# Performance work log

Hardware: AMD Instinct MI355X
Metric: run time of the kernel (lower is better)

## Reference

```python
import jax, jax.numpy as jnp
import numpy as np

H = 2048          # hidden_size
I_MOE = 1408      # moe_intermediate_size (per expert)
I_SH = 5632       # shared_expert_intermediate_size
E = 8             # num_experts
TOP_K = 2         # num_experts_per_tok
B, S = 1, 2048


def setup_inputs() -> dict:
    key = jax.random.key(0)
    ks = jax.random.split(key, 7)
    sc = 0.02
    return {
        "hidden_states": jax.random.normal(ks[0], (B, S, H), jnp.float32),
        "W_router": jax.random.normal(ks[1], (E, H), jnp.float32) * sc,      # gate.weight
        "W_sgate": jax.random.normal(ks[2], (1, H), jnp.float32) * sc,       # shared_expert_gate.weight
        "Ws_gate_up": jax.random.normal(ks[3], (H, 2 * I_SH), jnp.float32) * sc,  # shared expert merged gate/up
        "Ws_down": jax.random.normal(ks[4], (I_SH, H), jnp.float32) * sc,
        "We_gate_up": jax.random.normal(ks[5], (E, H, 2 * I_MOE), jnp.float32) * sc,  # stacked expert gate/up
        "We_down": jax.random.normal(ks[6], (E, I_MOE, H), jnp.float32) * sc,
    }


def _silu_and_mul(gu, inter):
    # gate_up layout: [..., 2*inter] -> silu(gate) * up, matching SiluAndMul
    return jax.nn.silu(gu[..., :inter]) * gu[..., inter:]


def reference(hidden_states, W_router, W_sgate, Ws_gate_up, Ws_down, We_gate_up, We_down):
    orig_shape = hidden_states.shape
    x = hidden_states.reshape(-1, H)                     # [T, H]
    T = x.shape[0]

    # --- router: softmax in fp32 then top-k (NOT renormalized, as in source) ---
    logits = x @ W_router.T                              # [T, E]
    probs = jax.nn.softmax(logits.astype(jnp.float32), axis=-1)
    rw, sel = jax.lax.top_k(probs, TOP_K)                # [T, K]
    rw = rw.astype(x.dtype)

    # sparse combine matrix [T, E]: routing weight where selected, else 0
    combine = jnp.zeros((T, E), x.dtype).at[jnp.arange(T)[:, None], sel].add(rw)

    # --- shared expert ---
    sh = _silu_and_mul(x @ Ws_gate_up, I_SH) @ Ws_down    # [T, H]
    shared_out = sh * jax.nn.sigmoid(x @ W_sgate.T)       # [T, H]

    # --- experts: dense dispatch (math-identical to gather/MLP/index_add loop) ---
    gu = jnp.einsum('th,ehi->eti', x, We_gate_up)         # [E, T, 2*I_MOE]
    h = _silu_and_mul(gu, I_MOE)                          # [E, T, I_MOE]
    eo = jnp.einsum('eti,eih->eth', h, We_down)           # [E, T, H]
    sparse_out = jnp.einsum('eth,te->th', eo, combine)    # [T, H]

    return (shared_out + sparse_out).reshape(orig_shape)
```

## Files before the change

### kernel.cpp

```cpp
#include <hip/hip_runtime.h>
#include <cstdio>


#define H_DIM 2048
#define IMOE  1408
#define ISH   5632
#define NEXP  8
#define T_TOK 2048
#define TK_TOT (T_TOK * 2)

typedef __attribute__((ext_vector_type(8))) short short8;
typedef __attribute__((ext_vector_type(8))) __bf16 bf16x8;
typedef __attribute__((ext_vector_type(4))) float f32x4;

__device__ __forceinline__ float bf2f(unsigned short u) {
  union { unsigned int i; float f; } v; v.i = ((unsigned int)u) << 16; return v.f;
}
__device__ __forceinline__ unsigned short f2bf(float f) {
  union { float f; unsigned int i; } v; v.f = f;
  unsigned int x = v.i;
  return (unsigned short)((x + 0x7fffu + ((x >> 16) & 1u)) >> 16);
}

__device__ __forceinline__ f32x4 MFMA16(short8 a, short8 b, f32x4 c) {
  return __builtin_amdgcn_mfma_f32_16x16x32_bf16(
      __builtin_bit_cast(bf16x8, a), __builtin_bit_cast(bf16x8, b), c, 0, 0, 0);
}

__device__ __forceinline__ void gload_lds16(const unsigned short* g, unsigned short* l) {
  __builtin_amdgcn_global_load_lds(
      (const __attribute__((address_space(1))) unsigned int*)g,
      (__attribute__((address_space(3))) unsigned int*)l, 16, 0, 0);
}

__device__ __forceinline__ float silu_f(float x) { return x / (1.0f + __expf(-x)); }

#define SBAR()   asm volatile("s_barrier" ::: "memory")
#define VMCNT(n) asm volatile("s_waitcnt vmcnt(" #n ")" ::: "memory")


template <bool ILV>
__global__ __launch_bounds__(256)
void transpose_cvt_kernel(const float* __restrict__ src, unsigned short* __restrict__ dst,
                          int R, int C, int I, long sStride, long dStride) {
  src += (long)blockIdx.z * sStride;
  dst += (long)blockIdx.z * dStride;
  __shared__ float tile[32][33];
  int tx = threadIdx.x, ty = threadIdx.y;
  int x = blockIdx.x * 32 + tx;
  int yb = blockIdx.y * 32;
#pragma unroll
  for (int j = 0; j < 4; j++) {
    int y = yb + ty + j * 8;
    tile[ty + j * 8][tx] = src[(long)y * C + x];
  }
  __syncthreads();
  int r = yb + tx;
#pragma unroll
  for (int j = 0; j < 4; j++) {
    int c = blockIdx.x * 32 + ty + j * 8;
    int cd = ILV ? (c < I ? 2 * c : 2 * (c - I) + 1) : c;
    dst[(long)cd * R + r] = f2bf(tile[tx][ty + j * 8]);
  }
}

__global__ __launch_bounds__(256)
void cvt_x_kernel(const float* __restrict__ x, unsigned short* __restrict__ xb, int total4) {
  int i = blockIdx.x * 256 + threadIdx.x;
  if (i >= total4) return;
  float4 v = ((const float4*)x)[i];
  ushort4 o;
  o.x = f2bf(v.x); o.y = f2bf(v.y); o.z = f2bf(v.z); o.w = f2bf(v.w);
  ((ushort4*)xb)[i] = o;
}


__global__ __launch_bounds__(256)
void router_kernel(const float* __restrict__ x, const float* __restrict__ Wr,
                   const float* __restrict__ Wsg, float* __restrict__ rw,
                   int* __restrict__ sel, float* __restrict__ sgate_sig,
                   int* __restrict__ counts) {
  int t = blockIdx.x;
  const float* xr = x + (long)t * H_DIM;
  float p[9];
#pragma unroll
  for (int e = 0; e < 9; e++) p[e] = 0.0f;
  for (int h = threadIdx.x; h < H_DIM; h += 256) {
    float xv = xr[h];
#pragma unroll
    for (int e = 0; e < 8; e++) p[e] += xv * Wr[e * H_DIM + h];
    p[8] += xv * Wsg[h];
  }
#pragma unroll
  for (int e = 0; e < 9; e++)
    for (int off = 32; off > 0; off >>= 1)
      p[e] += __shfl_down(p[e], off, 64);
  __shared__ float red[4][9];
  int wave = threadIdx.x >> 6, lane = threadIdx.x & 63;
  if (lane == 0) {
#pragma unroll
    for (int e = 0; e < 9; e++) red[wave][e] = p[e];
  }
  __syncthreads();
  if (threadIdx.x == 0) {
    float lg[9];
#pragma unroll
    for (int e = 0; e < 9; e++) lg[e] = red[0][e] + red[1][e] + red[2][e] + red[3][e];
    float m = lg[0];
#pragma unroll
    for (int e = 1; e < 8; e++) m = fmaxf(m, lg[e]);
    float pr[8], s = 0.0f;
#pragma unroll
    for (int e = 0; e < 8; e++) { pr[e] = expf(lg[e] - m); s += pr[e]; }
    float inv = 1.0f / s;
#pragma unroll
    for (int e = 0; e < 8; e++) pr[e] *= inv;
    int i0 = 0;
#pragma unroll
    for (int e = 1; e < 8; e++) if (pr[e] > pr[i0]) i0 = e;
    int i1 = (i0 == 0) ? 1 : 0;
#pragma unroll
    for (int e = 0; e < 8; e++) if (e != i0 && pr[e] > pr[i1]) i1 = e;
    rw[t * 2] = pr[i0]; rw[t * 2 + 1] = pr[i1];
    sel[t * 2] = i0;    sel[t * 2 + 1] = i1;
    sgate_sig[t] = 1.0f / (1.0f + expf(-lg[8]));
    atomicAdd(&counts[i0], 1);
    atomicAdd(&counts[i1], 1);
  }
}

__global__ void scan_kernel(const int* __restrict__ counts, int* __restrict__ offsets) {
  if (threadIdx.x == 0 && blockIdx.x == 0) {
    int s = 0;
    for (int e = 0; e < NEXP; e++) { offsets[e] = s; s += counts[e]; }
    offsets[NEXP] = s;
  }
}

__global__ __launch_bounds__(256)
void scatter_kernel(const int* __restrict__ sel, const int* __restrict__ offsets,
                    int* __restrict__ cursor, int* __restrict__ tok_of_slot,
                    int* __restrict__ slot_of_tok) {
  int t = blockIdx.x * 256 + threadIdx.x;
  if (t >= T_TOK) return;
#pragma unroll
  for (int k = 0; k < 2; k++) {
    int e = sel[t * 2 + k];
    int pos = atomicAdd(&cursor[e], 1);
    int slot = offsets[e] + pos;
    tok_of_slot[slot] = t;
    slot_of_tok[t * 2 + k] = slot;
  }
}

__global__ __launch_bounds__(256)
void gather_kernel(const unsigned short* __restrict__ xbf, const int* __restrict__ tok,
                   unsigned short* __restrict__ xg) {
  int i = blockIdx.x * 256 + threadIdx.x;
  int slot = i >> 8, c8 = i & 255;
  long src = (long)tok[slot] * H_DIM + c8 * 8;
  ulonglong2 v = *(const ulonglong2*)(xbf + src);
  ((ulonglong2*)xg)[i] = v;
}

template <int EPI, bool EXPERT, bool GATHER>
__global__ __launch_bounds__(512, 2)
void gemm8_kernel(const unsigned short* __restrict__ A,
                  const unsigned short* __restrict__ BT,
                  void* __restrict__ Cv,
                  int N, int Kld, int KLEN, int M,
                  const int* __restrict__ counts, const int* __restrict__ offsets,
                  const int* __restrict__ tok_of_slot,
                  const float* __restrict__ rowscale, long bt_estride) {
  __shared__ unsigned short lds8[65536];

  int cnt = M, rowbase = 0, k0 = 0;
  const unsigned short* bt = BT;
  if constexpr (EXPERT) {
    int e = blockIdx.z;
    cnt = counts[e];
    rowbase = offsets[e];
    bt += (long)e * bt_estride;
  } else {
    k0 = blockIdx.z * KLEN;
  }
  int row0 = blockIdx.x * 256;
  if (row0 >= cnt) return;
  int col0 = blockIdx.y * 256;

  int tid = threadIdx.x, wave = tid >> 6, lane = tid & 63;
  int NT = KLEN / 32;

  const unsigned short* aSrc[2];
  const unsigned short* bSrc[2];
#pragma unroll
  for (int i = 0; i < 2; i++) {
    int r = i * 128 + (tid >> 2);
    int sw = (((tid & 3) ^ ((r >> 1) & 3)) * 8);
    long arow;
    if constexpr (EXPERT) {
      int s = rowbase + min(row0 + r, cnt - 1);
      arow = GATHER ? tok_of_slot[s] : s;
    } else {
      arow = row0 + r;
    }
    aSrc[i] = A + arow * (long)Kld + k0 + sw;
    bSrc[i] = bt + (long)(col0 + r) * Kld + k0 + sw;
  }
  int dA0 = wave * 512, dA1 = 4096 + wave * 512;
  int dB0 = 8192 + wave * 512, dB1 = 12288 + wave * 512;

  auto STAGE_A = [&](int u) {
    int b2 = (u & 3) * 16384;
    long kk = (long)min(u, NT - 1) * 32;
    gload_lds16(aSrc[0] + kk, &lds8[b2 + dA0]);
    gload_lds16(aSrc[1] + kk, &lds8[b2 + dA1]);
  };
  auto STAGE_B = [&](int u) {
    int b2 = (u & 3) * 16384;
    long kk = (long)min(u, NT - 1) * 32;
    gload_lds16(bSrc[0] + kk, &lds8[b2 + dB0]);
    gload_lds16(bSrc[1] + kk, &lds8[b2 + dB1]);
  };

  int wr = wave >> 2, wc = wave & 3;
  int fr = lane & 15, fg = lane >> 4;
  int addrA0[4], addrA1[4], addrB[4];
#pragma unroll
  for (int m = 0; m < 4; m++) {
    int rl0 = wr * 128 + m * 16 + fr;
    int rl1 = rl0 + 64;
    int cl  = wc * 64 + m * 16 + fr;
    addrA0[m] = rl0 * 32 + ((fg ^ ((rl0 >> 1) & 3)) * 8);
    addrA1[m] = rl1 * 32 + ((fg ^ ((rl1 >> 1) & 3)) * 8);
    addrB[m]  = 8192 + cl * 32 + ((fg ^ ((cl >> 1) & 3)) * 8);
  }

  STAGE_A(0); STAGE_B(0);
  STAGE_A(1); STAGE_B(1);
  STAGE_A(2); STAGE_B(2);
  VMCNT(8);
  SBAR();

  f32x4 acc[8][4] = {};

  for (int t = 0; t < NT; t++) {
    int b = (t & 3) * 16384;
    int u = t + 3;
    short8 Bf[4], Af[4];
#pragma unroll
    for (int n = 0; n < 4; n++) Bf[n] = *(const short8*)&lds8[b + addrB[n]];
#pragma unroll
    for (int m = 0; m < 4; m++) Af[m] = *(const short8*)&lds8[b + addrA0[m]];
    STAGE_A(u);
    SBAR();
    __builtin_amdgcn_s_setprio(1);
#pragma unroll
    for (int m = 0; m < 4; m++)
#pragma unroll
      for (int n = 0; n < 4; n++)
        acc[m][n] = MFMA16(Af[m], Bf[n], acc[m][n]);
    __builtin_amdgcn_s_setprio(0);
    SBAR();
#pragma unroll
    for (int m = 0; m < 4; m++) Af[m] = *(const short8*)&lds8[b + addrA1[m]];
    STAGE_B(u);
    SBAR();
    __builtin_amdgcn_s_setprio(1);
#pragma unroll
    for (int m = 0; m < 4; m++)
#pragma unroll
      for (int n = 0; n < 4; n++)
        acc[4 + m][n] = MFMA16(Af[m], Bf[n], acc[4 + m][n]);
    __builtin_amdgcn_s_setprio(0);
    VMCNT(8);
    SBAR();
  }
  VMCNT(0);

  int rowguard = cnt - row0;
#pragma unroll
  for (int mq = 0; mq < 8; mq++) {
    int rl = wr * 128 + (mq >> 2) * 64 + (mq & 3) * 16 + fg * 4;
#pragma unroll
    for (int n = 0; n < 4; n++) {
      int cg = col0 + wc * 64 + n * 16 + fr;
      f32x4 v = acc[mq][n];
#pragma unroll
      for (int j = 0; j < 4; j++) {
        int r = rl + j;
        float pv = __shfl_xor(v[j], 1);
        if (r < rowguard) {
          long orow = (long)rowbase + row0 + r;
          if constexpr (EPI == 1) {
            unsafeAtomicAdd(&((float*)Cv)[orow * (long)N + cg], v[j] * rowscale[orow]);
          } else if constexpr (EPI == 2) {
            ((float*)Cv)[orow * (long)N + cg] = v[j];
          } else {
            if (!(fr & 1)) {
              float hval = silu_f(v[j]) * pv;
              ((unsigned short*)Cv)[orow * (long)(N >> 1) + (cg >> 1)] = f2bf(hval);
            }
          }
        }
      }
    }
  }
}


__global__ __launch_bounds__(256)
void combine_kernel(float* __restrict__ out, const float* __restrict__ eo,
                    const int* __restrict__ slot_of_tok, const float* __restrict__ rw) {
  int i = blockIdx.x * 256 + threadIdx.x;
  const int h4n = H_DIM / 4;
  if (i >= T_TOK * h4n) return;
  int t = i / h4n;
  int h4 = i - t * h4n;
  int s0 = slot_of_tok[t * 2], s1 = slot_of_tok[t * 2 + 1];
  float w0 = rw[t * 2], w1 = rw[t * 2 + 1];
  float4 o = ((float4*)out)[i];
  float4 a = ((const float4*)eo)[(long)s0 * h4n + h4];
  float4 b = ((const float4*)eo)[(long)s1 * h4n + h4];
  o.x += w0 * a.x + w1 * b.x;
  o.y += w0 * a.y + w1 * b.y;
  o.z += w0 * a.z + w1 * b.z;
  o.w += w0 * a.w + w1 * b.w;
  ((float4*)out)[i] = o;
}


extern "C" void kernel_launch(void* const* d_in, const int* in_sizes, int n_in,
                              void* d_out, int out_size, void* d_ws, size_t ws_size,
                              hipStream_t stream) {
  (void)in_sizes; (void)n_in; (void)out_size;
  const float* x    = (const float*)d_in[0];
  const float* Wr   = (const float*)d_in[1];
  const float* Wsg  = (const float*)d_in[2];
  const float* Wsgu = (const float*)d_in[3];
  const float* Wsd  = (const float*)d_in[4];
  const float* Wegu = (const float*)d_in[5];
  const float* Wed  = (const float*)d_in[6];
  float* out = (float*)d_out;

  char* ws = (char*)d_ws;
  size_t off = 0;
  auto alloc = [&](size_t b) { size_t o = off; off += (b + 255) & ~(size_t)255; return o; };

  size_t o_xbf   = alloc((size_t)T_TOK * H_DIM * 2);
  size_t o_WsguT = alloc((size_t)2 * ISH * H_DIM * 2);
  size_t o_WsdT  = alloc((size_t)H_DIM * ISH * 2);
  size_t o_WeguT = alloc((size_t)NEXP * 2 * IMOE * H_DIM * 2);
  size_t o_WedT  = alloc((size_t)NEXP * H_DIM * IMOE * 2);
  size_t o_hsh   = alloc((size_t)T_TOK * ISH * 2);
  size_t o_he    = alloc((size_t)TK_TOT * IMOE * 2);
  size_t o_xg    = alloc((size_t)TK_TOT * H_DIM * 2);
  size_t o_ints  = alloc(256);
  size_t o_rw    = alloc((size_t)TK_TOT * 4);
  size_t o_sel   = alloc((size_t)TK_TOT * 4);
  size_t o_sg    = alloc((size_t)T_TOK * 4);
  size_t o_tok   = alloc((size_t)TK_TOT * 4);
  size_t o_s2t   = alloc((size_t)TK_TOT * 4);

  if (off > ws_size) {
    fprintf(stderr, "[moe kernel] workspace too small: need %zu have %zu\n", off, ws_size);
    return;
  }

  unsigned short* xbf   = (unsigned short*)(ws + o_xbf);
  unsigned short* WsguT = (unsigned short*)(ws + o_WsguT);
  unsigned short* WsdT  = (unsigned short*)(ws + o_WsdT);
  unsigned short* WeguT = (unsigned short*)(ws + o_WeguT);
  unsigned short* WedT  = (unsigned short*)(ws + o_WedT);
  unsigned short* h_sh  = (unsigned short*)(ws + o_hsh);
  unsigned short* h_e   = (unsigned short*)(ws + o_he);
  unsigned short* xg    = (unsigned short*)(ws + o_xg);
  float* eo             = (float*)(ws + o_WsguT);

  int* ints    = (int*)(ws + o_ints);
  int* counts  = ints;
  int* cursor  = ints + 8;
  int* offsets = ints + 16;
  float* rw    = (float*)(ws + o_rw);
  int* sel     = (int*)(ws + o_sel);
  float* sgate = (float*)(ws + o_sg);
  int* tok     = (int*)(ws + o_tok);
  int* s2t     = (int*)(ws + o_s2t);

  dim3 tb(32, 8, 1);

  hipMemsetAsync(ints, 0, 64, stream);
  hipMemsetAsync(out, 0, (size_t)T_TOK * H_DIM * 4, stream);

  transpose_cvt_kernel<true><<<dim3(2 * ISH / 32, H_DIM / 32, 1), tb, 0, stream>>>(
      Wsgu, WsguT, H_DIM, 2 * ISH, ISH, 0, 0);
  transpose_cvt_kernel<false><<<dim3(H_DIM / 32, ISH / 32, 1), tb, 0, stream>>>(
      Wsd, WsdT, ISH, H_DIM, 0, 0, 0);
  transpose_cvt_kernel<true><<<dim3(2 * IMOE / 32, H_DIM / 32, NEXP), tb, 0, stream>>>(
      Wegu, WeguT, H_DIM, 2 * IMOE, IMOE, (long)H_DIM * 2 * IMOE, (long)2 * IMOE * H_DIM);
  transpose_cvt_kernel<false><<<dim3(H_DIM / 32, IMOE / 32, NEXP), tb, 0, stream>>>(
      Wed, WedT, IMOE, H_DIM, 0, (long)IMOE * H_DIM, (long)H_DIM * IMOE);

  cvt_x_kernel<<<(T_TOK * H_DIM / 4) / 256, 256, 0, stream>>>(x, xbf, T_TOK * H_DIM / 4);

  router_kernel<<<T_TOK, 256, 0, stream>>>(x, Wr, Wsg, rw, sel, sgate, counts);
  scan_kernel<<<1, 64, 0, stream>>>(counts, offsets);
  scatter_kernel<<<(T_TOK + 255) / 256, 256, 0, stream>>>(sel, offsets, cursor, tok, s2t);
  gather_kernel<<<TK_TOT, 256, 0, stream>>>(xbf, tok, xg);

  gemm8_kernel<3, false, false><<<dim3(T_TOK / 256, 2 * ISH / 256, 1), 512, 0, stream>>>(
      xbf, WsguT, h_sh, 2 * ISH, H_DIM, H_DIM, T_TOK,
      nullptr, nullptr, nullptr, nullptr, 0);

  gemm8_kernel<3, true, false><<<dim3(T_TOK / 256, 2 * IMOE / 256, NEXP), 512, 0, stream>>>(
      xg, WeguT, h_e, 2 * IMOE, H_DIM, H_DIM, 0,
      counts, offsets, nullptr, nullptr, (long)2 * IMOE * H_DIM);

  gemm8_kernel<1, false, false><<<dim3(T_TOK / 256, H_DIM / 256, 4), 512, 0, stream>>>(
      h_sh, WsdT, out, H_DIM, ISH, ISH / 4, T_TOK,
      nullptr, nullptr, nullptr, sgate, 0);

  gemm8_kernel<2, true, false><<<dim3(T_TOK / 256, H_DIM / 256, NEXP), 512, 0, stream>>>(
      h_e, WedT, eo, H_DIM, IMOE, IMOE, 0,
      counts, offsets, nullptr, nullptr, (long)H_DIM * IMOE);

  combine_kernel<<<(T_TOK * H_DIM / 4) / 256, 256, 0, stream>>>(out, eo, s2t, rw);
}
```

Measured before the change: 797.5 us.

## Rewrite GEMM main loop as double-buffered BK=64 pipeline and interleave weight transposes

```diff
diff --git a/kernel.cpp b/kernel.cpp
--- a/kernel.cpp
+++ b/kernel.cpp
@@ -163,15 +163,14 @@
   ((ulonglong2*)xg)[i] = v;
 }
 
-template <int EPI, bool EXPERT, bool GATHER>
+template <int EPI, bool EXPERT>
 __global__ __launch_bounds__(512, 2)
-void gemm8_kernel(const unsigned short* __restrict__ A,
-                  const unsigned short* __restrict__ BT,
-                  void* __restrict__ Cv,
-                  int N, int Kld, int KLEN, int M,
-                  const int* __restrict__ counts, const int* __restrict__ offsets,
-                  const int* __restrict__ tok_of_slot,
-                  const float* __restrict__ rowscale, long bt_estride) {
+void gemm2p_kernel(const unsigned short* __restrict__ A,
+                   const unsigned short* __restrict__ BT,
+                   void* __restrict__ Cv,
+                   int N, int Kld, int KLEN, int M,
+                   const int* __restrict__ counts, const int* __restrict__ offsets,
+                   const float* __restrict__ rowscale, long bt_estride) {
   __shared__ unsigned short lds8[65536];
 
   int cnt = M, rowbase = 0, k0 = 0;
@@ -189,103 +188,75 @@
   int col0 = blockIdx.y * 256;
 
   int tid = threadIdx.x, wave = tid >> 6, lane = tid & 63;
-  int NT = KLEN / 32;
-
-  const unsigned short* aSrc[2];
-  const unsigned short* bSrc[2];
-#pragma unroll
-  for (int i = 0; i < 2; i++) {
-    int r = i * 128 + (tid >> 2);
-    int sw = (((tid & 3) ^ ((r >> 1) & 3)) * 8);
-    long arow;
-    if constexpr (EXPERT) {
-      int s = rowbase + min(row0 + r, cnt - 1);
-      arow = GATHER ? tok_of_slot[s] : s;
-    } else {
-      arow = row0 + r;
-    }
-    aSrc[i] = A + arow * (long)Kld + k0 + sw;
-    bSrc[i] = bt + (long)(col0 + r) * Kld + k0 + sw;
-  }
-  int dA0 = wave * 512, dA1 = 4096 + wave * 512;
-  int dB0 = 8192 + wave * 512, dB1 = 12288 + wave * 512;
-
-  auto STAGE_A = [&](int u) {
-    int b2 = (u & 3) * 16384;
-    long kk = (long)min(u, NT - 1) * 32;
-    gload_lds16(aSrc[0] + kk, &lds8[b2 + dA0]);
-    gload_lds16(aSrc[1] + kk, &lds8[b2 + dA1]);
-  };
-  auto STAGE_B = [&](int u) {
-    int b2 = (u & 3) * 16384;
-    long kk = (long)min(u, NT - 1) * 32;
-    gload_lds16(bSrc[0] + kk, &lds8[b2 + dB0]);
-    gload_lds16(bSrc[1] + kk, &lds8[b2 + dB1]);
-  };
+  int NT = KLEN / 64;
+
+  const unsigned short* aSrc[4];
+  const unsigned short* bSrc[4];
+#pragma unroll
+  for (int s = 0; s < 4; s++) {
+    int r = s * 64 + (tid >> 3);
+    int g = (tid & 7) ^ (r & 7);
+    long ar = row0 + r;
+    if (ar > cnt - 1) ar = cnt - 1;
+    ar += rowbase;
+    aSrc[s] = A + ar * (long)Kld + k0 + g * 8;
+    bSrc[s] = bt + (long)(col0 + r) * Kld + k0 + g * 8;
+  }
 
   int wr = wave >> 2, wc = wave & 3;
   int fr = lane & 15, fg = lane >> 4;
-  int addrA0[4], addrA1[4], addrB[4];
-#pragma unroll
-  for (int m = 0; m < 4; m++) {
-    int rl0 = wr * 128 + m * 16 + fr;
-    int rl1 = rl0 + 64;
-    int cl  = wc * 64 + m * 16 + fr;
-    addrA0[m] = rl0 * 32 + ((fg ^ ((rl0 >> 1) & 3)) * 8);
-    addrA1[m] = rl1 * 32 + ((fg ^ ((rl1 >> 1) & 3)) * 8);
-    addrB[m]  = 8192 + cl * 32 + ((fg ^ ((cl >> 1) & 3)) * 8);
-  }
-
-  STAGE_A(0); STAGE_B(0);
-  STAGE_A(1); STAGE_B(1);
-  STAGE_A(2); STAGE_B(2);
-  VMCNT(8);
+  int aOff[8][2], bOff[4][2];
+#pragma unroll
+  for (int ks = 0; ks < 2; ks++) {
+    int q = ((ks * 4 + fg) ^ (fr & 7)) * 8;
+#pragma unroll
+    for (int m = 0; m < 8; m++) aOff[m][ks] = (wr * 128 + m * 16 + fr) * 64 + q;
+#pragma unroll
+    for (int n = 0; n < 4; n++) bOff[n][ks] = (wc * 64 + n * 16 + fr) * 64 + q;
+  }
+
+#define STAGE(p, t) do { long kk = (long)(t) * 64; \
+    _Pragma("unroll") for (int s = 0; s < 4; s++) { \
+      gload_lds16(aSrc[s] + kk, &lds8[(p) * 16384 + s * 4096 + wave * 512]); \
+      gload_lds16(bSrc[s] + kk, &lds8[32768 + (p) * 16384 + s * 4096 + wave * 512]); \
+    } } while (0)
+
+  f32x4 acc[8][4] = {};
+
+  STAGE(0, 0);
+  VMCNT(0);
   SBAR();
 
-  f32x4 acc[8][4] = {};
-
   for (int t = 0; t < NT; t++) {
-    int b = (t & 3) * 16384;
-    int u = t + 3;
-    short8 Bf[4], Af[4];
-#pragma unroll
-    for (int n = 0; n < 4; n++) Bf[n] = *(const short8*)&lds8[b + addrB[n]];
-#pragma unroll
-    for (int m = 0; m < 4; m++) Af[m] = *(const short8*)&lds8[b + addrA0[m]];
-    STAGE_A(u);
+    int p = t & 1;
+    if (t + 1 < NT) STAGE(p ^ 1, t + 1);
+#pragma unroll
+    for (int ks = 0; ks < 2; ks++) {
+      short8 aF[8], bF[4];
+#pragma unroll
+      for (int m = 0; m < 8; m++) aF[m] = *(const short8*)&lds8[p * 16384 + aOff[m][ks]];
+#pragma unroll
+      for (int n = 0; n < 4; n++) bF[n] = *(const short8*)&lds8[32768 + p * 16384 + bOff[n][ks]];
+      __builtin_amdgcn_s_setprio(1);
+#pragma unroll
+      for (int m = 0; m < 8; m++)
+#pragma unroll
+        for (int n = 0; n < 4; n++)
+          acc[m][n] = MFMA16(aF[m], bF[n], acc[m][n]);
+      __builtin_amdgcn_s_setprio(0);
+    }
+    VMCNT(0);
     SBAR();
-    __builtin_amdgcn_s_setprio(1);
-#pragma unroll
-    for (int m = 0; m < 4; m++)
-#pragma unroll
-      for (int n = 0; n < 4; n++)
-        acc[m][n] = MFMA16(Af[m], Bf[n], acc[m][n]);
-    __builtin_amdgcn_s_setprio(0);
-    SBAR();
-#pragma unroll
-    for (int m = 0; m < 4; m++) Af[m] = *(const short8*)&lds8[b + addrA1[m]];
-    STAGE_B(u);
-    SBAR();
-    __builtin_amdgcn_s_setprio(1);
-#pragma unroll
-    for (int m = 0; m < 4; m++)
-#pragma unroll
-      for (int n = 0; n < 4; n++)
-        acc[4 + m][n] = MFMA16(Af[m], Bf[n], acc[4 + m][n]);
-    __builtin_amdgcn_s_setprio(0);
-    VMCNT(8);
-    SBAR();
-  }
-  VMCNT(0);
+  }
 
   int rowguard = cnt - row0;
 #pragma unroll
-  for (int mq = 0; mq < 8; mq++) {
-    int rl = wr * 128 + (mq >> 2) * 64 + (mq & 3) * 16 + fg * 4;
+  for (int m = 0; m < 8; m++) {
+    int rl = wr * 128 + m * 16 + fg * 4;
 #pragma unroll
     for (int n = 0; n < 4; n++) {
       int cg = col0 + wc * 64 + n * 16 + fr;
-      f32x4 v = acc[mq][n];
+      f32x4 v = acc[m][n];
 #pragma unroll
       for (int j = 0; j < 4; j++) {
         int r = rl + j;
@@ -306,6 +277,7 @@
       }
     }
   }
+#undef STAGE
 }
 
 
@@ -392,37 +364,34 @@
   hipMemsetAsync(ints, 0, 64, stream);
   hipMemsetAsync(out, 0, (size_t)T_TOK * H_DIM * 4, stream);
 
-  transpose_cvt_kernel<true><<<dim3(2 * ISH / 32, H_DIM / 32, 1), tb, 0, stream>>>(
-      Wsgu, WsguT, H_DIM, 2 * ISH, ISH, 0, 0);
-  transpose_cvt_kernel<false><<<dim3(H_DIM / 32, ISH / 32, 1), tb, 0, stream>>>(
-      Wsd, WsdT, ISH, H_DIM, 0, 0, 0);
-  transpose_cvt_kernel<true><<<dim3(2 * IMOE / 32, H_DIM / 32, NEXP), tb, 0, stream>>>(
-      Wegu, WeguT, H_DIM, 2 * IMOE, IMOE, (long)H_DIM * 2 * IMOE, (long)2 * IMOE * H_DIM);
-  transpose_cvt_kernel<false><<<dim3(H_DIM / 32, IMOE / 32, NEXP), tb, 0, stream>>>(
-      Wed, WedT, IMOE, H_DIM, 0, (long)IMOE * H_DIM, (long)H_DIM * IMOE);
-
   cvt_x_kernel<<<(T_TOK * H_DIM / 4) / 256, 256, 0, stream>>>(x, xbf, T_TOK * H_DIM / 4);
-
   router_kernel<<<T_TOK, 256, 0, stream>>>(x, Wr, Wsg, rw, sel, sgate, counts);
   scan_kernel<<<1, 64, 0, stream>>>(counts, offsets);
   scatter_kernel<<<(T_TOK + 255) / 256, 256, 0, stream>>>(sel, offsets, cursor, tok, s2t);
   gather_kernel<<<TK_TOT, 256, 0, stream>>>(xbf, tok, xg);
 
-  gemm8_kernel<3, false, false><<<dim3(T_TOK / 256, 2 * ISH / 256, 1), 512, 0, stream>>>(
-      xbf, WsguT, h_sh, 2 * ISH, H_DIM, H_DIM, T_TOK,
-      nullptr, nullptr, nullptr, nullptr, 0);
-
-  gemm8_kernel<3, true, false><<<dim3(T_TOK / 256, 2 * IMOE / 256, NEXP), 512, 0, stream>>>(
-      xg, WeguT, h_e, 2 * IMOE, H_DIM, H_DIM, 0,
-      counts, offsets, nullptr, nullptr, (long)2 * IMOE * H_DIM);
-
-  gemm8_kernel<1, false, false><<<dim3(T_TOK / 256, H_DIM / 256, 4), 512, 0, stream>>>(
-      h_sh, WsdT, out, H_DIM, ISH, ISH / 4, T_TOK,
-      nullptr, nullptr, nullptr, sgate, 0);
-
-  gemm8_kernel<2, true, false><<<dim3(T_TOK / 256, H_DIM / 256, NEXP), 512, 0, stream>>>(
-      h_e, WedT, eo, H_DIM, IMOE, IMOE, 0,
-      counts, offsets, nullptr, nullptr, (long)H_DIM * IMOE);
+
+  transpose_cvt_kernel<true><<<dim3(2 * ISH / 32, H_DIM / 32, 1), tb, 0, stream>>>(
+      Wsgu, WsguT, H_DIM, 2 * ISH, ISH, 0, 0);
+  gemm2p_kernel<3, false><<<dim3(T_TOK / 256, 2 * ISH / 256, 1), 512, 0, stream>>>(
+      xbf, WsguT, h_sh, 2 * ISH, H_DIM, H_DIM, T_TOK, nullptr, nullptr, nullptr, 0);
+
+  transpose_cvt_kernel<true><<<dim3(2 * IMOE / 32, H_DIM / 32, NEXP), tb, 0, stream>>>(
+      Wegu, WeguT, H_DIM, 2 * IMOE, IMOE, (long)H_DIM * 2 * IMOE, (long)2 * IMOE * H_DIM);
+  gemm2p_kernel<3, true><<<dim3(T_TOK / 256, 2 * IMOE / 256, NEXP), 512, 0, stream>>>(
+      xg, WeguT, h_e, 2 * IMOE, H_DIM, H_DIM, 0, counts, offsets, nullptr,
+      (long)2 * IMOE * H_DIM);
+
+  transpose_cvt_kernel<false><<<dim3(H_DIM / 32, ISH / 32, 1), tb, 0, stream>>>(
+      Wsd, WsdT, ISH, H_DIM, 0, 0, 0);
+  gemm2p_kernel<1, false><<<dim3(T_TOK / 256, H_DIM / 256, 4), 512, 0, stream>>>(
+      h_sh, WsdT, out, H_DIM, ISH, ISH / 4, T_TOK, nullptr, nullptr, sgate, 0);
+
+  transpose_cvt_kernel<false><<<dim3(H_DIM / 32, IMOE / 32, NEXP), tb, 0, stream>>>(
+      Wed, WedT, IMOE, H_DIM, 0, (long)IMOE * H_DIM, (long)H_DIM * IMOE);
+  gemm2p_kernel<2, true><<<dim3(T_TOK / 256, H_DIM / 256, NEXP), 512, 0, stream>>>(
+      h_e, WedT, eo, H_DIM, IMOE, IMOE, 0, counts, offsets, nullptr,
+      (long)H_DIM * IMOE);
 
   combine_kernel<<<(T_TOK * H_DIM / 4) / 256, 256, 0, stream>>>(out, eo, s2t, rw);
 }
```

New measurement: 775.9 us. 2.7% less time.
